# Kernel tuning notes

Hardware: AMD Instinct MI355X
Metric: run time of the kernel (lower is better)

## Reference

```python
import jax, jax.numpy as jnp
import numpy as np

B, N, D_IN, D_OUT = 8, 2048, 1024, 1024


def setup_inputs() -> dict:
    key = jax.random.key(0)
    k0, k1, k2, k3 = jax.random.split(key, 4)
    scale = 1.0 / np.sqrt(D_IN)
    x = jax.random.normal(k0, (B, N, D_IN), dtype=jnp.float32)
    Wq = jax.random.normal(k1, (D_IN, D_OUT), dtype=jnp.float32) * scale
    Wk = jax.random.normal(k2, (D_IN, D_OUT), dtype=jnp.float32) * scale
    Wv = jax.random.normal(k3, (D_IN, D_OUT), dtype=jnp.float32) * scale
    return {"x": x, "Wq": Wq, "Wk": Wk, "Wv": Wv}


def reference(x, Wq, Wk, Wv):
    # x: [b, n, d_in]; single-head causal attention, dropout p=0 (eval).
    q = jnp.einsum('bnd,de->bne', x, Wq)
    k = jnp.einsum('bnd,de->bne', x, Wk)
    v = jnp.einsum('bnd,de->bne', x, Wv)
    n = x.shape[1]
    scores = jnp.einsum('bqe,bke->bqk', q, k)  # [b, n, n]
    causal_mask = jnp.triu(jnp.ones((n, n), dtype=bool), k=1)
    scores = jnp.where(causal_mask, -jnp.inf, scores)
    scale = 1.0 / jnp.sqrt(jnp.asarray(k.shape[-1], dtype=scores.dtype))
    attn = jax.nn.softmax(scores * scale, axis=-1)
    context = jnp.einsum('bqk,bke->bqe', attn, v)
    return context
```

## Files before the change

kernel.cpp:

```cpp
#include <hip/hip_runtime.h>


typedef unsigned short u16;
typedef __bf16 bf16x8 __attribute__((ext_vector_type(8)));
typedef float f32x4 __attribute__((ext_vector_type(4)));
typedef unsigned short u16x8 __attribute__((ext_vector_type(8)));
typedef unsigned short u16x4 __attribute__((ext_vector_type(4)));

static constexpr int BATCH = 8;
static constexpr int SEQ = 2048;
static constexpr int DIM = 1024;

static constexpr size_t SZ_XB = (size_t)BATCH * SEQ * DIM * 2;
static constexpr size_t SZ_W  = (size_t)DIM * DIM * 2;
static constexpr size_t OFF_XB  = 0;
static constexpr size_t OFF_WQT = OFF_XB + SZ_XB;
static constexpr size_t OFF_WKT = OFF_WQT + SZ_W;
static constexpr size_t OFF_WVT = OFF_WKT + SZ_W;
static constexpr size_t OFF_Q   = OFF_WVT + SZ_W;
static constexpr size_t OFF_K   = OFF_Q + SZ_XB;
static constexpr size_t OFF_VT  = OFF_K + SZ_XB;
static constexpr size_t OFF_E   = OFF_VT + SZ_XB;

__device__ __forceinline__ u16 f2b(float f) {
  unsigned u = __builtin_bit_cast(unsigned, f);
  u += 0x7fffu + ((u >> 16) & 1u);
  return (u16)(u >> 16);
}

__device__ __forceinline__ void gload16(const u16* g, u16* l) {
  __builtin_amdgcn_global_load_lds((__attribute__((address_space(1))) void*)g,
                                   (__attribute__((address_space(3))) void*)l, 16, 0, 0);
}

#define VWAIT(N) asm volatile("s_waitcnt vmcnt(" #N ")" ::: "memory")

__device__ __forceinline__ void barrier_raw() {
  __builtin_amdgcn_sched_barrier(0);
  __builtin_amdgcn_s_barrier();
  __builtin_amdgcn_sched_barrier(0);
}

__global__ __launch_bounds__(256) void cast_f32_bf16(const float* __restrict__ in,
                                                     u16* __restrict__ out) {
  const size_t i = ((size_t)blockIdx.x * 256 + threadIdx.x) * 8;
  float4 a = *(const float4*)(in + i);
  float4 b = *(const float4*)(in + i + 4);
  u16x8 o;
  o[0] = f2b(a.x); o[1] = f2b(a.y); o[2] = f2b(a.z); o[3] = f2b(a.w);
  o[4] = f2b(b.x); o[5] = f2b(b.y); o[6] = f2b(b.z); o[7] = f2b(b.w);
  *reinterpret_cast<u16x8*>(out + i) = o;
}

__global__ __launch_bounds__(256) void transpose_cast_w(const float* __restrict__ W,
                                                        u16* __restrict__ WT) {
  __shared__ float t[32][33];
  const int k0 = blockIdx.x * 32, n0 = blockIdx.y * 32;
  const int tx = threadIdx.x, ty = threadIdx.y;
#pragma unroll
  for (int dy = 0; dy < 32; dy += 8)
    t[ty + dy][tx] = W[(size_t)(k0 + ty + dy) * DIM + n0 + tx];
  __syncthreads();
#pragma unroll
  for (int dy = 0; dy < 32; dy += 8)
    WT[(size_t)(n0 + ty + dy) * DIM + k0 + tx] = f2b(t[tx][ty + dy]);
}

template <int MODE>
__global__ __launch_bounds__(512, 2) void gemm256(
    const u16* __restrict__ A, size_t sA, int lda,
    const u16* __restrict__ Bt, size_t sB, int ldb,
    void* __restrict__ C, size_t sC, int ldc,
    int Kdim, float scale) {
  const int bx = blockIdx.x, bz = blockIdx.z;
  const int by = (MODE == 3) ? (int)(gridDim.y - 1 - blockIdx.y) : (int)blockIdx.y;
  if (MODE == 2 && bx > by) return;
  const u16* Ab = A + (size_t)bz * sA;
  const u16* Bb = Bt + (size_t)bz * sB;
  const int rowTile = by * 256, colTile = bx * 256;
  int kmax = Kdim;
  if (MODE == 3) {
    int km = (by + 1) * 256;
    if (km < kmax) kmax = km;
  }
  const int NT = kmax >> 5;

  __shared__ __align__(16) u16 lds[4 * 16384];

  const int tid = threadIdx.x;
  const int w = tid >> 6, l = tid & 63;
  const int wm = w >> 2, wn = w & 3;
  const int lr = l & 15, quad = l >> 4;

  auto srow = [](int c) { int u = (c & 7) ^ ((c >> 3) & 7); return 2 * (c >> 3) + (u >> 2); };
  auto skq  = [](int c) { int u = (c & 7) ^ ((c >> 3) & 7); return u & 3; };
  const u16* pA0 = Ab + (size_t)(rowTile + srow(tid)) * lda + skq(tid) * 8;
  const u16* pA1 = Ab + (size_t)(rowTile + srow(tid + 512)) * lda + skq(tid + 512) * 8;
  const u16* pB0 = Bb + (size_t)(colTile + srow(tid)) * ldb + skq(tid) * 8;
  const u16* pB1 = Bb + (size_t)(colTile + srow(tid + 512)) * ldb + skq(tid + 512) * 8;

  int offA[8], offB[4];
#pragma unroll
  for (int mi = 0; mi < 8; ++mi) {
    const int row = wm * 128 + mi * 16 + lr;
    offA[mi] = ((row * 64 + quad * 16) ^ (((row >> 1) & 7) << 4)) >> 1;
  }
#pragma unroll
  for (int ni = 0; ni < 4; ++ni) {
    const int row = wn * 64 + ni * 16 + lr;
    offB[ni] = ((row * 64 + quad * 16) ^ (((row >> 1) & 7) << 4)) >> 1;
  }

  f32x4 acc[8][4];
#pragma unroll
  for (int i = 0; i < 8; ++i)
#pragma unroll
    for (int j = 0; j < 4; ++j) acc[i][j] = (f32x4){0.f, 0.f, 0.f, 0.f};
  float rsum[8] = {0.f, 0.f, 0.f, 0.f, 0.f, 0.f, 0.f, 0.f};

#define STAGE_B(tt)                               \
  {                                               \
    u16* sb = &lds[((tt) & 3) * 16384];           \
    const int ko = (tt) * 32;                     \
    gload16(pB0 + ko, sb + 8192 + w * 512);       \
    gload16(pB1 + ko, sb + 12288 + w * 512);      \
  }
#define STAGE_A(tt)                               \
  {                                               \
    u16* sb = &lds[((tt) & 3) * 16384];           \
    const int ko = (tt) * 32;                     \
    gload16(pA0 + ko, sb + w * 512);              \
    gload16(pA1 + ko, sb + 4096 + w * 512);       \
  }

  STAGE_B(0); STAGE_A(0);
  STAGE_B(1); STAGE_A(1);
  STAGE_B(2); STAGE_A(2);
  VWAIT(8);
  barrier_raw();

  for (int t = 0; t < NT; ++t) {
    const u16* As = &lds[(t & 3) * 16384];
    const u16* Bs = As + 8192;
    bf16x8 af[8], bf[4];

#pragma unroll
    for (int mi = 0; mi < 4; ++mi)
      af[mi] = *reinterpret_cast<const bf16x8*>(&As[offA[mi]]);
#pragma unroll
    for (int ni = 0; ni < 4; ++ni)
      bf[ni] = *reinterpret_cast<const bf16x8*>(&Bs[offB[ni]]);
    if (t + 3 < NT) STAGE_B(t + 3);
    barrier_raw();
    if (MODE == 3) {
#pragma unroll
      for (int mi = 0; mi < 4; ++mi) {
        float s = 0.f;
#pragma unroll
        for (int j = 0; j < 8; ++j) s += (float)af[mi][j];
        rsum[mi] += s;
      }
    }
    __builtin_amdgcn_s_setprio(1);
#pragma unroll
    for (int mi = 0; mi < 4; ++mi)
#pragma unroll
      for (int ni = 0; ni < 4; ++ni)
        acc[mi][ni] =
            __builtin_amdgcn_mfma_f32_16x16x32_bf16(af[mi], bf[ni], acc[mi][ni], 0, 0, 0);
    __builtin_amdgcn_s_setprio(0);

#pragma unroll
    for (int mi = 4; mi < 8; ++mi)
      af[mi] = *reinterpret_cast<const bf16x8*>(&As[offA[mi]]);
    if (t + 3 < NT) {
      STAGE_A(t + 3);
      VWAIT(8);
    } else if (t + 2 < NT) {
      VWAIT(4);
    } else if (t + 1 < NT) {
      VWAIT(0);
    }
    barrier_raw();
    if (MODE == 3) {
#pragma unroll
      for (int mi = 4; mi < 8; ++mi) {
        float s = 0.f;
#pragma unroll
        for (int j = 0; j < 8; ++j) s += (float)af[mi][j];
        rsum[mi] += s;
      }
    }
    __builtin_amdgcn_s_setprio(1);
#pragma unroll
    for (int mi = 4; mi < 8; ++mi)
#pragma unroll
      for (int ni = 0; ni < 4; ++ni)
        acc[mi][ni] =
            __builtin_amdgcn_mfma_f32_16x16x32_bf16(af[mi], bf[ni], acc[mi][ni], 0, 0, 0);
    __builtin_amdgcn_s_setprio(0);
  }
#undef STAGE_A
#undef STAGE_B

  if (MODE == 3) {
#pragma unroll
    for (int mi = 0; mi < 8; ++mi) {
      rsum[mi] += __shfl_xor(rsum[mi], 16);
      rsum[mi] += __shfl_xor(rsum[mi], 32);
    }
  }

  const int orow0 = rowTile + wm * 128 + quad * 4;
  const int ocol0 = colTile + wn * 64 + lr;
#pragma unroll
  for (int mi = 0; mi < 8; ++mi) {
    float linv[4];
    if (MODE == 3) {
#pragma unroll
      for (int r = 0; r < 4; ++r) linv[r] = 1.f / __shfl(rsum[mi], quad * 4 + r);
    }
#pragma unroll
    for (int ni = 0; ni < 4; ++ni) {
      const int colg = ocol0 + ni * 16;
      if (MODE == 1) {
        const int rowg0 = orow0 + mi * 16;
        const int bb = rowg0 >> 11, nn = rowg0 & (SEQ - 1);
        u16x4 pk;
#pragma unroll
        for (int r = 0; r < 4; ++r) pk[r] = f2b(acc[mi][ni][r]);
        *reinterpret_cast<u16x4*>(&((u16*)C)[(size_t)bb * sC + (size_t)colg * ldc + nn]) = pk;
      } else {
#pragma unroll
        for (int r = 0; r < 4; ++r) {
          const int rowg = orow0 + mi * 16 + r;
          const float v = acc[mi][ni][r];
          if (MODE == 0) {
            ((u16*)C)[(size_t)bz * sC + (size_t)rowg * ldc + colg] = f2b(v);
          } else if (MODE == 2) {
            const float e = (colg <= rowg) ? __expf(v * scale) : 0.f;
            ((u16*)C)[(size_t)bz * sC + (size_t)rowg * ldc + colg] = f2b(e);
          } else {
            ((float*)C)[(size_t)bz * sC + (size_t)rowg * ldc + colg] = v * linv[r];
          }
        }
      }
    }
  }
}

extern "C" void kernel_launch(void* const* d_in, const int* in_sizes, int n_in,
                              void* d_out, int out_size, void* d_ws, size_t ws_size,
                              hipStream_t stream) {
  const float* x = (const float*)d_in[0];
  const float* Wq = (const float*)d_in[1];
  const float* Wk = (const float*)d_in[2];
  const float* Wv = (const float*)d_in[3];
  float* out = (float*)d_out;
  char* ws = (char*)d_ws;

  u16* xb = (u16*)(ws + OFF_XB);
  u16* wqT = (u16*)(ws + OFF_WQT);
  u16* wkT = (u16*)(ws + OFF_WKT);
  u16* wvT = (u16*)(ws + OFF_WVT);
  u16* qb = (u16*)(ws + OFF_Q);
  u16* kb = (u16*)(ws + OFF_K);
  u16* vt = (u16*)(ws + OFF_VT);
  u16* eb = (u16*)(ws + OFF_E);

  const int total = BATCH * SEQ * DIM;
  cast_f32_bf16<<<total / (256 * 8), 256, 0, stream>>>(x, xb);
  transpose_cast_w<<<dim3(32, 32), dim3(32, 8), 0, stream>>>(Wq, wqT);
  transpose_cast_w<<<dim3(32, 32), dim3(32, 8), 0, stream>>>(Wk, wkT);
  transpose_cast_w<<<dim3(32, 32), dim3(32, 8), 0, stream>>>(Wv, wvT);

  gemm256<0><<<dim3(4, 64, 1), 512, 0, stream>>>(xb, 0, DIM, wqT, 0, DIM, qb, 0, DIM,
                                                 DIM, 1.f);
  gemm256<0><<<dim3(4, 64, 1), 512, 0, stream>>>(xb, 0, DIM, wkT, 0, DIM, kb, 0, DIM,
                                                 DIM, 1.f);
  gemm256<1><<<dim3(4, 64, 1), 512, 0, stream>>>(xb, 0, DIM, wvT, 0, DIM, vt,
                                                 (size_t)DIM * SEQ, SEQ, DIM, 1.f);
  gemm256<2><<<dim3(8, 8, BATCH), 512, 0, stream>>>(
      qb, (size_t)SEQ * DIM, DIM, kb, (size_t)SEQ * DIM, DIM, eb, (size_t)SEQ * SEQ, SEQ,
      DIM, 0.03125f);
  gemm256<3><<<dim3(4, 8, BATCH), 512, 0, stream>>>(
      eb, (size_t)SEQ * SEQ, SEQ, vt, (size_t)DIM * SEQ, SEQ, out, (size_t)SEQ * DIM, DIM,
      SEQ, 1.f);
}
```

Baseline: 391.3 us.

## Shrink GEMM tiles to 128x256 with 3-stage pipeline and higher occupancy

Replaces the 256x256 tile GEMM with a 128x256 tile, halving per-wave accumulators and using a 3-buffer LDS ring instead of 4, with one barrier per k-step. Launch bounds move to 4 blocks per CU and the grids double in the row dimension, giving finer granularity for the causal-skipped QK^T and PV stages. The intent is better occupancy and less load imbalance on the triangular work. The cost is less data reuse per tile, since B is reloaded twice as often.

```diff
diff --git a/kernel.cpp b/kernel.cpp
--- a/kernel.cpp
+++ b/kernel.cpp
@@ -67,25 +67,25 @@
 }
 
 template <int MODE>
-__global__ __launch_bounds__(512, 2) void gemm256(
+__global__ __launch_bounds__(512, 4) void gemm128(
     const u16* __restrict__ A, size_t sA, int lda,
     const u16* __restrict__ Bt, size_t sB, int ldb,
     void* __restrict__ C, size_t sC, int ldc,
     int Kdim, float scale) {
   const int bx = blockIdx.x, bz = blockIdx.z;
   const int by = (MODE == 3) ? (int)(gridDim.y - 1 - blockIdx.y) : (int)blockIdx.y;
-  if (MODE == 2 && bx > by) return;
+  if (MODE == 2 && 2 * bx > by) return;
   const u16* Ab = A + (size_t)bz * sA;
   const u16* Bb = Bt + (size_t)bz * sB;
-  const int rowTile = by * 256, colTile = bx * 256;
+  const int rowTile = by * 128, colTile = bx * 256;
   int kmax = Kdim;
   if (MODE == 3) {
-    int km = (by + 1) * 256;
+    int km = (by + 1) * 128;
     if (km < kmax) kmax = km;
   }
   const int NT = kmax >> 5;
 
-  __shared__ __align__(16) u16 lds[4 * 16384];
+  __shared__ __align__(16) u16 lds[3 * 12288];
 
   const int tid = threadIdx.x;
   const int w = tid >> 6, l = tid & 63;
@@ -95,63 +95,52 @@
   auto srow = [](int c) { int u = (c & 7) ^ ((c >> 3) & 7); return 2 * (c >> 3) + (u >> 2); };
   auto skq  = [](int c) { int u = (c & 7) ^ ((c >> 3) & 7); return u & 3; };
   const u16* pA0 = Ab + (size_t)(rowTile + srow(tid)) * lda + skq(tid) * 8;
-  const u16* pA1 = Ab + (size_t)(rowTile + srow(tid + 512)) * lda + skq(tid + 512) * 8;
   const u16* pB0 = Bb + (size_t)(colTile + srow(tid)) * ldb + skq(tid) * 8;
   const u16* pB1 = Bb + (size_t)(colTile + srow(tid + 512)) * ldb + skq(tid + 512) * 8;
 
-  int offA[8], offB[4];
-#pragma unroll
-  for (int mi = 0; mi < 8; ++mi) {
-    const int row = wm * 128 + mi * 16 + lr;
+  int offA[4], offB[4];
+#pragma unroll
+  for (int mi = 0; mi < 4; ++mi) {
+    const int row = wm * 64 + mi * 16 + lr;
     offA[mi] = ((row * 64 + quad * 16) ^ (((row >> 1) & 7) << 4)) >> 1;
   }
 #pragma unroll
   for (int ni = 0; ni < 4; ++ni) {
     const int row = wn * 64 + ni * 16 + lr;
-    offB[ni] = ((row * 64 + quad * 16) ^ (((row >> 1) & 7) << 4)) >> 1;
-  }
-
-  f32x4 acc[8][4];
-#pragma unroll
-  for (int i = 0; i < 8; ++i)
+    offB[ni] = 4096 + ((((row * 64 + quad * 16) ^ (((row >> 1) & 7) << 4))) >> 1);
+  }
+
+  f32x4 acc[4][4];
+#pragma unroll
+  for (int i = 0; i < 4; ++i)
 #pragma unroll
     for (int j = 0; j < 4; ++j) acc[i][j] = (f32x4){0.f, 0.f, 0.f, 0.f};
-  float rsum[8] = {0.f, 0.f, 0.f, 0.f, 0.f, 0.f, 0.f, 0.f};
-
-#define STAGE_B(tt)                               \
-  {                                               \
-    u16* sb = &lds[((tt) & 3) * 16384];           \
-    const int ko = (tt) * 32;                     \
-    gload16(pB0 + ko, sb + 8192 + w * 512);       \
-    gload16(pB1 + ko, sb + 12288 + w * 512);      \
-  }
-#define STAGE_A(tt)                               \
-  {                                               \
-    u16* sb = &lds[((tt) & 3) * 16384];           \
-    const int ko = (tt) * 32;                     \
-    gload16(pA0 + ko, sb + w * 512);              \
-    gload16(pA1 + ko, sb + 4096 + w * 512);       \
-  }
-
-  STAGE_B(0); STAGE_A(0);
-  STAGE_B(1); STAGE_A(1);
-  STAGE_B(2); STAGE_A(2);
-  VWAIT(8);
+  float rsum[4] = {0.f, 0.f, 0.f, 0.f};
+
+#define STAGE(tt)                                   \
+  {                                                 \
+    u16* sb = &lds[((unsigned)(tt) % 3u) * 12288];  \
+    const int ko = (tt) * 32;                       \
+    gload16(pA0 + ko, sb + w * 512);                \
+    gload16(pB0 + ko, sb + 4096 + w * 512);         \
+    gload16(pB1 + ko, sb + 8192 + w * 512);         \
+  }
+
+  STAGE(0);
+  STAGE(1);
+  VWAIT(3);
   barrier_raw();
 
   for (int t = 0; t < NT; ++t) {
-    const u16* As = &lds[(t & 3) * 16384];
-    const u16* Bs = As + 8192;
-    bf16x8 af[8], bf[4];
-
+    const u16* S = &lds[((unsigned)t % 3u) * 12288];
+    bf16x8 af[4], bf[4];
 #pragma unroll
     for (int mi = 0; mi < 4; ++mi)
-      af[mi] = *reinterpret_cast<const bf16x8*>(&As[offA[mi]]);
+      af[mi] = *reinterpret_cast<const bf16x8*>(&S[offA[mi]]);
 #pragma unroll
     for (int ni = 0; ni < 4; ++ni)
-      bf[ni] = *reinterpret_cast<const bf16x8*>(&Bs[offB[ni]]);
-    if (t + 3 < NT) STAGE_B(t + 3);
-    barrier_raw();
+      bf[ni] = *reinterpret_cast<const bf16x8*>(&S[offB[ni]]);
+    if (t + 2 < NT) STAGE(t + 2);
     if (MODE == 3) {
 #pragma unroll
       for (int mi = 0; mi < 4; ++mi) {
@@ -169,52 +158,28 @@
         acc[mi][ni] =
             __builtin_amdgcn_mfma_f32_16x16x32_bf16(af[mi], bf[ni], acc[mi][ni], 0, 0, 0);
     __builtin_amdgcn_s_setprio(0);
-
-#pragma unroll
-    for (int mi = 4; mi < 8; ++mi)
-      af[mi] = *reinterpret_cast<const bf16x8*>(&As[offA[mi]]);
-    if (t + 3 < NT) {
-      STAGE_A(t + 3);
-      VWAIT(8);
-    } else if (t + 2 < NT) {
-      VWAIT(4);
+    if (t + 2 < NT) {
+      VWAIT(3);
     } else if (t + 1 < NT) {
       VWAIT(0);
     }
+    asm volatile("s_waitcnt lgkmcnt(0)" ::: "memory");
     barrier_raw();
-    if (MODE == 3) {
-#pragma unroll
-      for (int mi = 4; mi < 8; ++mi) {
-        float s = 0.f;
-#pragma unroll
-        for (int j = 0; j < 8; ++j) s += (float)af[mi][j];
-        rsum[mi] += s;
-      }
-    }
-    __builtin_amdgcn_s_setprio(1);
-#pragma unroll
-    for (int mi = 4; mi < 8; ++mi)
-#pragma unroll
-      for (int ni = 0; ni < 4; ++ni)
-        acc[mi][ni] =
-            __builtin_amdgcn_mfma_f32_16x16x32_bf16(af[mi], bf[ni], acc[mi][ni], 0, 0, 0);
-    __builtin_amdgcn_s_setprio(0);
-  }
-#undef STAGE_A
-#undef STAGE_B
+  }
+#undef STAGE
 
   if (MODE == 3) {
 #pragma unroll
-    for (int mi = 0; mi < 8; ++mi) {
+    for (int mi = 0; mi < 4; ++mi) {
       rsum[mi] += __shfl_xor(rsum[mi], 16);
       rsum[mi] += __shfl_xor(rsum[mi], 32);
     }
   }
 
-  const int orow0 = rowTile + wm * 128 + quad * 4;
+  const int orow0 = rowTile + wm * 64 + quad * 4;
   const int ocol0 = colTile + wn * 64 + lr;
 #pragma unroll
-  for (int mi = 0; mi < 8; ++mi) {
+  for (int mi = 0; mi < 4; ++mi) {
     float linv[4];
     if (MODE == 3) {
 #pragma unroll
@@ -274,16 +239,16 @@
   transpose_cast_w<<<dim3(32, 32), dim3(32, 8), 0, stream>>>(Wk, wkT);
   transpose_cast_w<<<dim3(32, 32), dim3(32, 8), 0, stream>>>(Wv, wvT);
 
-  gemm256<0><<<dim3(4, 64, 1), 512, 0, stream>>>(xb, 0, DIM, wqT, 0, DIM, qb, 0, DIM,
-                                                 DIM, 1.f);
-  gemm256<0><<<dim3(4, 64, 1), 512, 0, stream>>>(xb, 0, DIM, wkT, 0, DIM, kb, 0, DIM,
-                                                 DIM, 1.f);
-  gemm256<1><<<dim3(4, 64, 1), 512, 0, stream>>>(xb, 0, DIM, wvT, 0, DIM, vt,
-                                                 (size_t)DIM * SEQ, SEQ, DIM, 1.f);
-  gemm256<2><<<dim3(8, 8, BATCH), 512, 0, stream>>>(
+  gemm128<0><<<dim3(4, 128, 1), 512, 0, stream>>>(xb, 0, DIM, wqT, 0, DIM, qb, 0, DIM,
+                                                  DIM, 1.f);
+  gemm128<0><<<dim3(4, 128, 1), 512, 0, stream>>>(xb, 0, DIM, wkT, 0, DIM, kb, 0, DIM,
+                                                  DIM, 1.f);
+  gemm128<1><<<dim3(4, 128, 1), 512, 0, stream>>>(xb, 0, DIM, wvT, 0, DIM, vt,
+                                                  (size_t)DIM * SEQ, SEQ, DIM, 1.f);
+  gemm128<2><<<dim3(8, 16, BATCH), 512, 0, stream>>>(
       qb, (size_t)SEQ * DIM, DIM, kb, (size_t)SEQ * DIM, DIM, eb, (size_t)SEQ * SEQ, SEQ,
       DIM, 0.03125f);
-  gemm256<3><<<dim3(4, 8, BATCH), 512, 0, stream>>>(
+  gemm128<3><<<dim3(4, 16, BATCH), 512, 0, stream>>>(
       eb, (size_t)SEQ * SEQ, SEQ, vt, (size_t)DIM * SEQ, SEQ, out, (size_t)SEQ * DIM, DIM,
       SEQ, 1.f);
 }
```

New measurement: 392.7 us. About the same (+0.4%).
